# Kernel optimization log

Hardware: AMD Instinct MI355X
Metric: run time of the kernel (lower is better)

The kernel has to match this reference:

```python
import jax, jax.numpy as jnp
import numpy as np

N, M = 50000, 16
NODE_DIM, EDGE_DIM = 128, 64
CONCAT_DIM = 2 * NODE_DIM + EDGE_DIM  # 320
LN_EPS = 1e-6  # flax.linen.LayerNorm default


def setup_inputs() -> dict:
    key = jax.random.key(0)
    ks = jax.random.split(key, 5)
    x = jax.random.normal(ks[0], (N, NODE_DIM), dtype=jnp.float32)
    nbr_fea = jax.random.normal(ks[1], (N, M, EDGE_DIM), dtype=jnp.float32)
    nbr_fea_idx = jax.random.randint(ks[2], (N, M), 0, N)
    ln_scale = jnp.ones((NODE_DIM,), dtype=jnp.float32)
    ln_bias = jnp.zeros((NODE_DIM,), dtype=jnp.float32)
    # lecun_normal-ish init scaled by fan-in (flax Dense default is lecun_normal)
    W1 = jax.random.normal(ks[3], (CONCAT_DIM, NODE_DIM), dtype=jnp.float32) / np.sqrt(CONCAT_DIM)
    b1 = jnp.zeros((NODE_DIM,), dtype=jnp.float32)
    W2 = jax.random.normal(ks[4], (NODE_DIM, NODE_DIM), dtype=jnp.float32) / np.sqrt(NODE_DIM)
    b2 = jnp.zeros((NODE_DIM,), dtype=jnp.float32)
    return {"x": x, "nbr_fea": nbr_fea, "nbr_fea_idx": nbr_fea_idx,
            "ln_scale": ln_scale, "ln_bias": ln_bias,
            "W1": W1, "b1": b1, "W2": W2, "b2": b2}


def _layer_norm(x, scale, bias):
    mu = jnp.mean(x, axis=-1, keepdims=True)
    var = jnp.mean(jnp.square(x - mu), axis=-1, keepdims=True)
    return (x - mu) * jax.lax.rsqrt(var + LN_EPS) * scale + bias


def reference(x, nbr_fea, nbr_fea_idx, ln_scale, ln_bias, W1, b1, W2, b2):
    # x: [N, D], nbr_fea: [N, M, E], nbr_fea_idx: [N, M]
    x_normed = _layer_norm(x, ln_scale, ln_bias)                 # [N, D]
    x_nbr = jnp.take(x_normed, nbr_fea_idx, axis=0)              # [N, M, D]
    m = nbr_fea_idx.shape[1]
    x_center = jnp.broadcast_to(x_normed[:, None, :], (x.shape[0], m, x.shape[1]))
    concat = jnp.concatenate([x_center, x_nbr, nbr_fea], axis=-1)  # [N, M, 2D+E]
    h = jax.nn.silu(jnp.einsum('nmc,cd->nmd', concat, W1) + b1)   # [N, M, D]
    msg = jnp.einsum('nmd,de->nme', h, W2) + b2                   # [N, M, D]
    agg = jnp.sum(msg, axis=1)                                    # [N, D]
    return x + agg
```

## Files before the change

### kernel.cpp

```cpp
#include <hip/hip_runtime.h>
#include <math.h>

#define N_NODES 50000
#define M_NBR 16
#define D 128
#define E 64

typedef __attribute__((ext_vector_type(8))) __bf16 bf16x8;
typedef __attribute__((ext_vector_type(4))) float f32x4;

__device__ __forceinline__ void gload16(const void* g, void* l) {
  __builtin_amdgcn_global_load_lds(
      (const __attribute__((address_space(1))) void*)g,
      (__attribute__((address_space(3))) void*)l, 16, 0, 0);
}

__device__ __forceinline__ int swz(int o) { return o ^ (((o >> 7) & 7) << 4); }


__global__ __launch_bounds__(256) void k_prep(const float* __restrict__ W1,
                                              const float* __restrict__ W2,
                                              __bf16* __restrict__ w1a_f,
                                              __bf16* __restrict__ w1b_f,
                                              __bf16* __restrict__ w1c_f,
                                              __bf16* __restrict__ w2_f) {
  const int t = blockIdx.x * 256 + threadIdx.x;
  if (t < 16384) {
    const int j = t & 7, r = (t >> 3) & 15, c = (t >> 7) & 3, q = t >> 9;
    const int kt = q & 3, dt = q >> 2;
    w1a_f[t] = (__bf16)W1[(kt * 32 + c * 8 + j) * 128 + dt * 16 + r];
  } else if (t < 32768) {
    const int u = t - 16384;
    const int j = u & 7, r = (u >> 3) & 15, c = (u >> 7) & 3, q = u >> 9;
    const int kt = q & 3, dt = q >> 2;
    w1b_f[u] = (__bf16)W1[(128 + kt * 32 + c * 8 + j) * 128 + dt * 16 + r];
  } else if (t < 40960) {
    const int u = t - 32768;
    const int j = u & 7, r = (u >> 3) & 15, c = (u >> 7) & 3, q = u >> 9;
    const int kt = q & 1, dt = q >> 1;
    w1c_f[u] = (__bf16)W1[(256 + kt * 32 + c * 8 + j) * 128 + dt * 16 + r];
  } else if (t < 57344) {
    const int u = t - 40960;
    const int j = u & 7, r = (u >> 3) & 15, c = (u >> 7) & 3, q = u >> 9;
    const int kt = q & 3, dt = q >> 2;
    w2_f[u] = (__bf16)W2[(kt * 32 + c * 8 + j) * 128 + dt * 16 + r];
  }
}

__global__ __launch_bounds__(256) void k_t12f(const float* __restrict__ x,
                                              const float* __restrict__ sc,
                                              const float* __restrict__ bi,
                                              const __bf16* __restrict__ w1a_f,
                                              const __bf16* __restrict__ w1b_f,
                                              const float* __restrict__ b1,
                                              __bf16* __restrict__ t1bp,
                                              __bf16* __restrict__ t2bp) {
  const int wave = blockIdx.x * 4 + (threadIdx.x >> 6);
  if (wave >= N_NODES / 16) return;
  const int lane = threadIdx.x & 63;
  const int r = lane & 15, c = lane >> 4;
  const int node0 = wave * 16;

  const float* row = x + (size_t)(node0 + r) * 128 + c * 8;
  f32x4 va[8];
  #pragma unroll
  for (int kt = 0; kt < 4; ++kt) {
    va[2 * kt]     = *(const f32x4*)(row + kt * 32);
    va[2 * kt + 1] = *(const f32x4*)(row + kt * 32 + 4);
  }
  float s = 0.f;
  #pragma unroll
  for (int q = 0; q < 8; ++q) s += va[q][0] + va[q][1] + va[q][2] + va[q][3];
  s += __shfl_xor(s, 16, 64);
  s += __shfl_xor(s, 32, 64);
  const float mu = s * (1.0f / 128.0f);
  float qs = 0.f;
  #pragma unroll
  for (int q = 0; q < 8; ++q) {
    #pragma unroll
    for (int e = 0; e < 4; ++e) { const float dxx = va[q][e] - mu; qs += dxx * dxx; }
  }
  qs += __shfl_xor(qs, 16, 64);
  qs += __shfl_xor(qs, 32, 64);
  const float rs = rsqrtf(qs * (1.0f / 128.0f) + 1e-6f);

  bf16x8 af[4];
  #pragma unroll
  for (int kt = 0; kt < 4; ++kt) {
    const f32x4 s_lo = *(const f32x4*)(sc + kt * 32 + c * 8);
    const f32x4 s_hi = *(const f32x4*)(sc + kt * 32 + c * 8 + 4);
    const f32x4 b_lo = *(const f32x4*)(bi + kt * 32 + c * 8);
    const f32x4 b_hi = *(const f32x4*)(bi + kt * 32 + c * 8 + 4);
    #pragma unroll
    for (int e = 0; e < 4; ++e) {
      af[kt][e]     = (__bf16)(((va[2 * kt][e]     - mu) * rs) * s_lo[e] + b_lo[e]);
      af[kt][4 + e] = (__bf16)(((va[2 * kt + 1][e] - mu) * rs) * s_hi[e] + b_hi[e]);
    }
  }

  const bf16x8* wa = (const bf16x8*)w1a_f;
  const bf16x8* wb = (const bf16x8*)w1b_f;
  f32x4 acc1[8], acc2[8];
  #pragma unroll
  for (int dt = 0; dt < 8; ++dt) { acc1[dt] = (f32x4){0,0,0,0}; acc2[dt] = (f32x4){0,0,0,0}; }
  #pragma unroll
  for (int dt = 0; dt < 8; ++dt) {
    #pragma unroll
    for (int kt = 0; kt < 4; ++kt) {
      const bf16x8 bfa = wa[(dt * 4 + kt) * 64 + c * 16 + r];
      acc1[dt] = __builtin_amdgcn_mfma_f32_16x16x32_bf16(af[kt], bfa, acc1[dt], 0, 0, 0);
      const bf16x8 bfb = wb[(dt * 4 + kt) * 64 + c * 16 + r];
      acc2[dt] = __builtin_amdgcn_mfma_f32_16x16x32_bf16(af[kt], bfb, acc2[dt], 0, 0, 0);
    }
  }

  float b1v[8];
  #pragma unroll
  for (int dt = 0; dt < 8; ++dt) b1v[dt] = b1[dt * 16 + r];
  #pragma unroll
  for (int j = 0; j < 4; ++j) {
    const int node = node0 + c * 4 + j;
    bf16x8 t1v, t2v;
    #pragma unroll
    for (int dt = 0; dt < 8; ++dt) {
      t1v[dt] = (__bf16)(acc1[dt][j] + b1v[dt]);
      t2v[dt] = (__bf16)acc2[dt][j];
    }
    *(bf16x8*)(t1bp + (size_t)node * 128 + r * 8) = t1v;
    *(bf16x8*)(t2bp + (size_t)node * 128 + r * 8) = t2v;
  }
}

#define HPITCH 136

__global__ __launch_bounds__(256, 4) void k_edge2(const float* __restrict__ nbr,
                                                  const int* __restrict__ idx,
                                                  const __bf16* __restrict__ t1bp,
                                                  const __bf16* __restrict__ t2bp,
                                                  const __bf16* __restrict__ w1c_f,
                                                  const __bf16* __restrict__ w2_f,
                                                  const float* __restrict__ b2,
                                                  const float* __restrict__ x,
                                                  float* __restrict__ out) {
  __shared__ __bf16 wlds[8192];
  __shared__ __bf16 hlds[16 * HPITCH];
  const int lane = threadIdx.x & 63;
  const int wid  = threadIdx.x >> 6;
  const int r = lane & 15, c = lane >> 4;
  const int nb0 = blockIdx.x * 16;

  {
    const int s0 = wid * 1024 + lane * 16;
    #pragma unroll
    for (int q = 0; q < 4; ++q) {
      const int s = s0 + q * 4096;
      gload16((const char*)w1c_f + swz(s), (char*)wlds + s);
    }
  }
  __syncthreads();

  #pragma unroll
  for (int i = 0; i < 4; ++i) {
    const int row = wid * 4 + i;
    const int n = nb0 + row;

    const int4 g = *(const int4*)(idx + n * M_NBR + c * 4);
    const float* arow = nbr + (size_t)n * (M_NBR * E) + r * E + c * 8;
    const f32x4 a0 = *(const f32x4*)(arow);
    const f32x4 a1 = *(const f32x4*)(arow + 4);
    const f32x4 a2 = *(const f32x4*)(arow + 32);
    const f32x4 a3 = *(const f32x4*)(arow + 36);
    const bf16x8 t1v = *(const bf16x8*)(t1bp + (size_t)n * 128 + r * 8);
    const bf16x8 tg0 = *(const bf16x8*)(t2bp + (size_t)g.x * 128 + r * 8);
    const bf16x8 tg1 = *(const bf16x8*)(t2bp + (size_t)g.y * 128 + r * 8);
    const bf16x8 tg2 = *(const bf16x8*)(t2bp + (size_t)g.z * 128 + r * 8);
    const bf16x8 tg3 = *(const bf16x8*)(t2bp + (size_t)g.w * 128 + r * 8);

    bf16x8 af0, af1;
    #pragma unroll
    for (int e = 0; e < 4; ++e) {
      af0[e] = (__bf16)a0[e]; af0[4 + e] = (__bf16)a1[e];
      af1[e] = (__bf16)a2[e]; af1[4 + e] = (__bf16)a3[e];
    }

    f32x4 acc[8];
    #pragma unroll
    for (int dt = 0; dt < 8; ++dt) acc[dt] = (f32x4){0, 0, 0, 0};
    #pragma unroll
    for (int dt = 0; dt < 8; ++dt) {
      const int o0 = ((dt * 2 + 0) * 64 + c * 16 + r) * 16;
      const int o1 = ((dt * 2 + 1) * 64 + c * 16 + r) * 16;
      const bf16x8 b0 = *(const bf16x8*)((const char*)wlds + swz(o0));
      const bf16x8 b1 = *(const bf16x8*)((const char*)wlds + swz(o1));
      acc[dt] = __builtin_amdgcn_mfma_f32_16x16x32_bf16(af0, b0, acc[dt], 0, 0, 0);
      acc[dt] = __builtin_amdgcn_mfma_f32_16x16x32_bf16(af1, b1, acc[dt], 0, 0, 0);
    }

    #pragma unroll
    for (int dt = 0; dt < 8; ++dt) {
      const float tb = (float)t1v[dt];
      float s = 0.f;
      { const float h = acc[dt][0] + tb + (float)tg0[dt]; s += __fdividef(h, 1.0f + __expf(-h)); }
      { const float h = acc[dt][1] + tb + (float)tg1[dt]; s += __fdividef(h, 1.0f + __expf(-h)); }
      { const float h = acc[dt][2] + tb + (float)tg2[dt]; s += __fdividef(h, 1.0f + __expf(-h)); }
      { const float h = acc[dt][3] + tb + (float)tg3[dt]; s += __fdividef(h, 1.0f + __expf(-h)); }
      s += __shfl_xor(s, 16, 64);
      s += __shfl_xor(s, 32, 64);
      if (lane < 16) hlds[row * HPITCH + dt * 16 + lane] = (__bf16)s;
    }
  }
  __syncthreads();

  const int dtA = wid * 2, dtB = wid * 2 + 1;
  const bf16x8* w2 = (const bf16x8*)w2_f;
  bf16x8 bA[4], bB[4];
  #pragma unroll
  for (int kt = 0; kt < 4; ++kt) {
    bA[kt] = w2[(dtA * 4 + kt) * 64 + c * 16 + r];
    bB[kt] = w2[(dtB * 4 + kt) * 64 + c * 16 + r];
  }
  bf16x8 haf[4];
  #pragma unroll
  for (int kt = 0; kt < 4; ++kt)
    haf[kt] = *(const bf16x8*)(hlds + r * HPITCH + kt * 32 + c * 8);

  f32x4 accA = (f32x4){0,0,0,0}, accB = (f32x4){0,0,0,0};
  #pragma unroll
  for (int kt = 0; kt < 4; ++kt) {
    accA = __builtin_amdgcn_mfma_f32_16x16x32_bf16(haf[kt], bA[kt], accA, 0, 0, 0);
    accB = __builtin_amdgcn_mfma_f32_16x16x32_bf16(haf[kt], bB[kt], accB, 0, 0, 0);
  }

  const float b2A = 16.0f * b2[dtA * 16 + r];
  const float b2B = 16.0f * b2[dtB * 16 + r];
  #pragma unroll
  for (int j = 0; j < 4; ++j) {
    const int node = nb0 + c * 4 + j;
    const size_t oA = (size_t)node * 128 + dtA * 16 + r;
    const size_t oB = (size_t)node * 128 + dtB * 16 + r;
    out[oA] = x[oA] + accA[j] + b2A;
    out[oB] = x[oB] + accB[j] + b2B;
  }
}

extern "C" void kernel_launch(void* const* d_in, const int* in_sizes, int n_in,
                              void* d_out, int out_size, void* d_ws, size_t ws_size,
                              hipStream_t stream) {
  const float* x        = (const float*)d_in[0];
  const float* nbr_fea  = (const float*)d_in[1];
  const int*   nbr_idx  = (const int*)d_in[2];
  const float* ln_scale = (const float*)d_in[3];
  const float* ln_bias  = (const float*)d_in[4];
  const float* W1       = (const float*)d_in[5];
  const float* b1       = (const float*)d_in[6];
  const float* W2       = (const float*)d_in[7];
  const float* b2       = (const float*)d_in[8];
  float* out = (float*)d_out;

  char* ws = (char*)d_ws;
  __bf16* t1bp   = (__bf16*)(ws);
  __bf16* t2bp   = (__bf16*)(ws + 12800000);
  __bf16* w1a_f  = (__bf16*)(ws + 25600000);
  __bf16* w1b_f  = (__bf16*)(ws + 25632768);
  __bf16* w1c_f  = (__bf16*)(ws + 25665536);
  __bf16* w2_f   = (__bf16*)(ws + 25681920);

  k_prep  <<<224, 256, 0, stream>>>(W1, W2, w1a_f, w1b_f, w1c_f, w2_f);
  k_t12f  <<<(N_NODES / 16 + 3) / 4, 256, 0, stream>>>(x, ln_scale, ln_bias,
                                                       w1a_f, w1b_f, b1, t1bp, t2bp);
  k_edge2 <<<N_NODES / 16, 256, 0, stream>>>(nbr_fea, nbr_idx, t1bp, t2bp,
                                             w1c_f, w2_f, b2, x, out);
}
```

Measured before the change: 120.0 us.

## Software-pipeline per-node loads in edge kernel with double-buffered registers

Restructures the per-wave loop over four nodes into a two-deep software pipeline: neighbor-feature and gathered t2 loads for the next node are issued before computing the current one, with compiler memory fences pinning the order. Index loads are hoisted to overlap the weight LDS prefetch before the barrier. This aims to hide global and gather latency behind MFMA and SiLU work, at the cost of more live registers, so launch bounds drop from 4 to 3 blocks per CU, lowering occupancy.

```diff
diff --git a/kernel.cpp b/kernel.cpp
--- a/kernel.cpp
+++ b/kernel.cpp
@@ -14,6 +14,8 @@
       (const __attribute__((address_space(1))) void*)g,
       (__attribute__((address_space(3))) void*)l, 16, 0, 0);
 }
+
+#define FENCE() asm volatile("" ::: "memory")
 
 __device__ __forceinline__ int swz(int o) { return o ^ (((o >> 7) & 7) << 4); }
 
@@ -133,7 +135,66 @@
 
 #define HPITCH 136
 
-__global__ __launch_bounds__(256, 4) void k_edge2(const float* __restrict__ nbr,
+struct NL {
+  f32x4 a0, a1, a2, a3;
+  bf16x8 t1v;
+  bf16x8 tg0, tg1, tg2, tg3;
+};
+
+__device__ __forceinline__ NL load_node(const float* __restrict__ nbr,
+                                        const __bf16* __restrict__ t1bp,
+                                        const __bf16* __restrict__ t2bp,
+                                        int n, int4 g, int r, int c) {
+  NL v;
+  const float* arow = nbr + (size_t)n * (M_NBR * E) + r * E + c * 8;
+  v.a0 = *(const f32x4*)(arow);
+  v.a1 = *(const f32x4*)(arow + 4);
+  v.a2 = *(const f32x4*)(arow + 32);
+  v.a3 = *(const f32x4*)(arow + 36);
+  v.t1v = *(const bf16x8*)(t1bp + (size_t)n * 128 + r * 8);
+  v.tg0 = *(const bf16x8*)(t2bp + (size_t)g.x * 128 + r * 8);
+  v.tg1 = *(const bf16x8*)(t2bp + (size_t)g.y * 128 + r * 8);
+  v.tg2 = *(const bf16x8*)(t2bp + (size_t)g.z * 128 + r * 8);
+  v.tg3 = *(const bf16x8*)(t2bp + (size_t)g.w * 128 + r * 8);
+  return v;
+}
+
+__device__ __forceinline__ void compute_node(const NL& v, const __bf16* wlds,
+                                             __bf16* hlds, int row,
+                                             int lane, int r, int c) {
+  bf16x8 af0, af1;
+  #pragma unroll
+  for (int e = 0; e < 4; ++e) {
+    af0[e] = (__bf16)v.a0[e]; af0[4 + e] = (__bf16)v.a1[e];
+    af1[e] = (__bf16)v.a2[e]; af1[4 + e] = (__bf16)v.a3[e];
+  }
+  f32x4 acc[8];
+  #pragma unroll
+  for (int dt = 0; dt < 8; ++dt) acc[dt] = (f32x4){0, 0, 0, 0};
+  #pragma unroll
+  for (int dt = 0; dt < 8; ++dt) {
+    const int o0 = ((dt * 2 + 0) * 64 + c * 16 + r) * 16;
+    const int o1 = ((dt * 2 + 1) * 64 + c * 16 + r) * 16;
+    const bf16x8 b0 = *(const bf16x8*)((const char*)wlds + swz(o0));
+    const bf16x8 b1 = *(const bf16x8*)((const char*)wlds + swz(o1));
+    acc[dt] = __builtin_amdgcn_mfma_f32_16x16x32_bf16(af0, b0, acc[dt], 0, 0, 0);
+    acc[dt] = __builtin_amdgcn_mfma_f32_16x16x32_bf16(af1, b1, acc[dt], 0, 0, 0);
+  }
+  #pragma unroll
+  for (int dt = 0; dt < 8; ++dt) {
+    const float tb = (float)v.t1v[dt];
+    float s = 0.f;
+    { const float h = acc[dt][0] + tb + (float)v.tg0[dt]; s += __fdividef(h, 1.0f + __expf(-h)); }
+    { const float h = acc[dt][1] + tb + (float)v.tg1[dt]; s += __fdividef(h, 1.0f + __expf(-h)); }
+    { const float h = acc[dt][2] + tb + (float)v.tg2[dt]; s += __fdividef(h, 1.0f + __expf(-h)); }
+    { const float h = acc[dt][3] + tb + (float)v.tg3[dt]; s += __fdividef(h, 1.0f + __expf(-h)); }
+    s += __shfl_xor(s, 16, 64);
+    s += __shfl_xor(s, 32, 64);
+    if (lane < 16) hlds[row * HPITCH + dt * 16 + lane] = (__bf16)s;
+  }
+}
+
+__global__ __launch_bounds__(256, 3) void k_edge2(const float* __restrict__ nbr,
                                                   const int* __restrict__ idx,
                                                   const __bf16* __restrict__ t1bp,
                                                   const __bf16* __restrict__ t2bp,
@@ -148,6 +209,7 @@
   const int wid  = threadIdx.x >> 6;
   const int r = lane & 15, c = lane >> 4;
   const int nb0 = blockIdx.x * 16;
+  const int row0 = wid * 4;
 
   {
     const int s0 = wid * 1024 + lane * 16;
@@ -157,58 +219,28 @@
       gload16((const char*)w1c_f + swz(s), (char*)wlds + s);
     }
   }
+
+  const int4 g0 = *(const int4*)(idx + (nb0 + row0 + 0) * M_NBR + c * 4);
+  const int4 g1 = *(const int4*)(idx + (nb0 + row0 + 1) * M_NBR + c * 4);
+  const int4 g2 = *(const int4*)(idx + (nb0 + row0 + 2) * M_NBR + c * 4);
+  const int4 g3 = *(const int4*)(idx + (nb0 + row0 + 3) * M_NBR + c * 4);
+
   __syncthreads();
 
-  #pragma unroll
-  for (int i = 0; i < 4; ++i) {
-    const int row = wid * 4 + i;
-    const int n = nb0 + row;
-
-    const int4 g = *(const int4*)(idx + n * M_NBR + c * 4);
-    const float* arow = nbr + (size_t)n * (M_NBR * E) + r * E + c * 8;
-    const f32x4 a0 = *(const f32x4*)(arow);
-    const f32x4 a1 = *(const f32x4*)(arow + 4);
-    const f32x4 a2 = *(const f32x4*)(arow + 32);
-    const f32x4 a3 = *(const f32x4*)(arow + 36);
-    const bf16x8 t1v = *(const bf16x8*)(t1bp + (size_t)n * 128 + r * 8);
-    const bf16x8 tg0 = *(const bf16x8*)(t2bp + (size_t)g.x * 128 + r * 8);
-    const bf16x8 tg1 = *(const bf16x8*)(t2bp + (size_t)g.y * 128 + r * 8);
-    const bf16x8 tg2 = *(const bf16x8*)(t2bp + (size_t)g.z * 128 + r * 8);
-    const bf16x8 tg3 = *(const bf16x8*)(t2bp + (size_t)g.w * 128 + r * 8);
-
-    bf16x8 af0, af1;
-    #pragma unroll
-    for (int e = 0; e < 4; ++e) {
-      af0[e] = (__bf16)a0[e]; af0[4 + e] = (__bf16)a1[e];
-      af1[e] = (__bf16)a2[e]; af1[4 + e] = (__bf16)a3[e];
-    }
-
-    f32x4 acc[8];
-    #pragma unroll
-    for (int dt = 0; dt < 8; ++dt) acc[dt] = (f32x4){0, 0, 0, 0};
-    #pragma unroll
-    for (int dt = 0; dt < 8; ++dt) {
-      const int o0 = ((dt * 2 + 0) * 64 + c * 16 + r) * 16;
-      const int o1 = ((dt * 2 + 1) * 64 + c * 16 + r) * 16;
-      const bf16x8 b0 = *(const bf16x8*)((const char*)wlds + swz(o0));
-      const bf16x8 b1 = *(const bf16x8*)((const char*)wlds + swz(o1));
-      acc[dt] = __builtin_amdgcn_mfma_f32_16x16x32_bf16(af0, b0, acc[dt], 0, 0, 0);
-      acc[dt] = __builtin_amdgcn_mfma_f32_16x16x32_bf16(af1, b1, acc[dt], 0, 0, 0);
-    }
-
-    #pragma unroll
-    for (int dt = 0; dt < 8; ++dt) {
-      const float tb = (float)t1v[dt];
-      float s = 0.f;
-      { const float h = acc[dt][0] + tb + (float)tg0[dt]; s += __fdividef(h, 1.0f + __expf(-h)); }
-      { const float h = acc[dt][1] + tb + (float)tg1[dt]; s += __fdividef(h, 1.0f + __expf(-h)); }
-      { const float h = acc[dt][2] + tb + (float)tg2[dt]; s += __fdividef(h, 1.0f + __expf(-h)); }
-      { const float h = acc[dt][3] + tb + (float)tg3[dt]; s += __fdividef(h, 1.0f + __expf(-h)); }
-      s += __shfl_xor(s, 16, 64);
-      s += __shfl_xor(s, 32, 64);
-      if (lane < 16) hlds[row * HPITCH + dt * 16 + lane] = (__bf16)s;
-    }
-  }
+  NL va = load_node(nbr, t1bp, t2bp, nb0 + row0 + 0, g0, r, c);
+  NL vb = load_node(nbr, t1bp, t2bp, nb0 + row0 + 1, g1, r, c);
+  FENCE();
+  compute_node(va, wlds, hlds, row0 + 0, lane, r, c);
+
+  va = load_node(nbr, t1bp, t2bp, nb0 + row0 + 2, g2, r, c);
+  FENCE();
+  compute_node(vb, wlds, hlds, row0 + 1, lane, r, c);
+
+  vb = load_node(nbr, t1bp, t2bp, nb0 + row0 + 3, g3, r, c);
+  FENCE();
+  compute_node(va, wlds, hlds, row0 + 2, lane, r, c);
+  compute_node(vb, wlds, hlds, row0 + 3, lane, r, c);
+
   __syncthreads();
 
   const int dtA = wid * 2, dtB = wid * 2 + 1;
```

After: 114.7 us (median of 2 runs). 4.5% less time.
